# Performance work log

Hardware: AMD Instinct MI355X
Metric: run time of the kernel (lower is better)

## Reference

```python
import jax, jax.numpy as jnp
import numpy as np

N, E = 100000, 1600000
F_IN, F_HID, F_OUT = 64, 64, 16


def setup_inputs() -> dict:
    key = jax.random.key(0)
    ks = jax.random.split(key, 10)
    def g(k, shape):
        return jax.random.normal(k, shape, dtype=jnp.float32) * 0.05
    return {
        "x": jax.random.normal(ks[0], (N, F_IN), dtype=jnp.float32),
        "adj": jax.random.randint(ks[1], (2, E), 0, N, dtype=jnp.int32),
        # ChebConv K=2 params: per-order weights [in, out] + shared bias
        "W1_0": g(ks[2], (F_IN, F_HID)), "W1_1": g(ks[3], (F_IN, F_HID)),
        "b1": jnp.zeros((F_HID,), jnp.float32),
        "Wx_0": g(ks[4], (F_HID, F_HID)), "Wx_1": g(ks[5], (F_HID, F_HID)),
        "bx": jnp.zeros((F_HID,), jnp.float32),
        "W2_0": g(ks[6], (F_HID, F_OUT)), "W2_1": g(ks[7], (F_HID, F_OUT)),
        "b2": jnp.zeros((F_OUT,), jnp.float32),
    }


def _cheb(x, row, col, w, W0, W1, b):
    # K=2 Chebyshev conv: Tx0 = x, Tx1 = L_hat @ x (sparse propagate)
    n = x.shape[0]
    tx1 = jax.ops.segment_sum(w[:, None] * x[col], row, num_segments=n)
    return x @ W0 + tx1 @ W1 + b


def reference(x, adj, W1_0, W1_1, b1, Wx_0, Wx_1, bx, W2_0, W2_1, b2):
    row, col = adj[0], adj[1]
    n = x.shape[0]
    # sym-normalized Laplacian scaled by 2/lambda_max (=1): diagonal cancels,
    # off-diagonal weight = -deg^{-1/2}[row] * deg^{-1/2}[col]
    deg = jax.ops.segment_sum(jnp.ones(adj.shape[1], x.dtype), row, num_segments=n)
    dis = jnp.where(deg > 0, jax.lax.rsqrt(jnp.maximum(deg, 1e-12)), 0.0)
    w = -dis[row] * dis[col]
    h = jax.nn.relu(_cheb(x, row, col, w, W1_0, W1_1, b1))
    # dropout is identity in eval mode
    h = jax.nn.relu(_cheb(h, row, col, w, Wx_0, Wx_1, bx))
    return _cheb(h, row, col, w, W2_0, W2_1, b2)
```

## Files before the change

### kernel.cpp

```cpp
#include <hip/hip_runtime.h>
#include <hip/hip_bf16.h>


#define EPB 4096

typedef __attribute__((ext_vector_type(8))) short bf16x8;
typedef __attribute__((ext_vector_type(4))) float f32x4;

__device__ __forceinline__ float bf2f(unsigned short u) {
    unsigned int x = ((unsigned int)u) << 16;
    return __uint_as_float(x);
}
__device__ __forceinline__ unsigned short f2bf(float f) {
    unsigned int b = __float_as_uint(f);
    unsigned int r = (b + 0x7FFF + ((b >> 16) & 1)) >> 16;
    return (unsigned short)r;
}
__device__ __forceinline__ void acc8(float* a, bf16x8 v) {
#pragma unroll
    for (int i = 0; i < 8; ++i) a[i] += bf2f((unsigned short)(short)v[i]);
}
__device__ __forceinline__ void acc8m(float* a, bf16x8 v, bool m) {
#pragma unroll
    for (int i = 0; i < 8; ++i) a[i] += m ? bf2f((unsigned short)(short)v[i]) : 0.0f;
}

template <int NC>
__device__ __forceinline__ void pack_pair(const float* __restrict__ W0,
                                          const float* __restrict__ W1,
                                          unsigned short* __restrict__ out, int idx) {
    constexpr int NT = NC / 16;
    int i = idx & 7;
    int m = (idx >> 3) & 15;
    int g = (idx >> 7) & 3;
    int f = idx >> 9;
    int nt = f % NT;
    int kt = f / NT;
    const float* W = (kt < 2) ? W0 : W1;
    int k = (kt & 1) * 32 + g * 8 + i;
    out[idx] = f2bf(W[k * NC + nt * 16 + m]);
}

__global__ __launch_bounds__(256) void wconv_all(const float* __restrict__ W1_0,
                                                 const float* __restrict__ W1_1,
                                                 const float* __restrict__ Wx_0,
                                                 const float* __restrict__ Wx_1,
                                                 const float* __restrict__ W2_0,
                                                 const float* __restrict__ W2_1,
                                                 unsigned short* __restrict__ wp1,
                                                 unsigned short* __restrict__ wpx,
                                                 unsigned short* __restrict__ wp2,
                                                 int* __restrict__ bcnt, int nbk) {
    int idx = blockIdx.x * 256 + threadIdx.x;
    if (idx < nbk) bcnt[idx] = 0;
    if (idx < 8192) pack_pair<64>(W1_0, W1_1, wp1, idx);
    else if (idx < 16384) pack_pair<64>(Wx_0, Wx_1, wpx, idx - 8192);
    else if (idx < 18432) pack_pair<16>(W2_0, W2_1, wp2, idx - 16384);
}

__global__ __launch_bounds__(256) void bucket_count(const int* __restrict__ row,
                                                    int* __restrict__ bcnt,
                                                    int e, int nbk) {
    __shared__ int bh[512];
    int tid = threadIdx.x;
    for (int j = tid; j < nbk; j += 256) bh[j] = 0;
    __syncthreads();
    int base = blockIdx.x * EPB;
#pragma unroll
    for (int k = 0; k < EPB / 256; ++k) {
        int i = base + k * 256 + tid;
        if (i < e) atomicAdd(&bh[row[i] >> 8], 1);
    }
    __syncthreads();
    for (int j = tid; j < nbk; j += 256) {
        int c = bh[j];
        if (c) atomicAdd(&bcnt[j], c);
    }
}

__global__ __launch_bounds__(256) void bucket_scan(const int* __restrict__ bcnt,
                                                   int* __restrict__ bbase,
                                                   int* __restrict__ bcursor,
                                                   int* __restrict__ off,
                                                   int nbk, int n, int e) {
    __shared__ int sa[512], sb[512];
    int tid = threadIdx.x;
    for (int j = tid; j < 512; j += 256) sa[j] = (j < nbk) ? bcnt[j] : 0;
    __syncthreads();
    int* in = sa;
    int* out = sb;
    for (int d = 1; d < 512; d <<= 1) {
        for (int j = tid; j < 512; j += 256)
            out[j] = in[j] + ((j >= d) ? in[j - d] : 0);
        __syncthreads();
        int* t = in; in = out; out = t;
    }
    for (int j = tid; j < nbk; j += 256) {
        int incl = in[j];
        int excl = incl - bcnt[j];
        bbase[j] = excl;
        bcursor[j] = excl;
        if (j == nbk - 1) bbase[nbk] = incl;
    }
    if (tid == 0) off[n] = e;
}

__global__ __launch_bounds__(256) void bucket_scatter(const int* __restrict__ row,
                                                      const int* __restrict__ col,
                                                      int* __restrict__ bcursor,
                                                      int* __restrict__ packed,
                                                      int e, int nbk) {
    __shared__ int bh[512];
    __shared__ int bbase[512];
    __shared__ int bcur[512];
    int tid = threadIdx.x;
    for (int j = tid; j < nbk; j += 256) { bh[j] = 0; bcur[j] = 0; }
    __syncthreads();
    int base = blockIdx.x * EPB;
#pragma unroll
    for (int k = 0; k < EPB / 256; ++k) {
        int i = base + k * 256 + tid;
        if (i < e) atomicAdd(&bh[row[i] >> 8], 1);
    }
    __syncthreads();
    for (int j = tid; j < nbk; j += 256) {
        int c = bh[j];
        bbase[j] = c ? atomicAdd(&bcursor[j], c) : 0;
    }
    __syncthreads();
#pragma unroll
    for (int k = 0; k < EPB / 256; ++k) {
        int i = base + k * 256 + tid;
        if (i < e) {
            int r = row[i];
            int b = r >> 8;
            int slot = bbase[b] + atomicAdd(&bcur[b], 1);
            packed[slot] = ((r & 255) << 17) | col[i];
        }
    }
}

__global__ __launch_bounds__(256) void bucket_build(const int* __restrict__ packed,
                                                    const int* __restrict__ bbase,
                                                    const float* __restrict__ x,
                                                    int* __restrict__ off,
                                                    float* __restrict__ dis,
                                                    int* __restrict__ csr,
                                                    unsigned short* __restrict__ y,
                                                    unsigned short* __restrict__ xb,
                                                    int n) {
    __shared__ int rcnt[256];
    __shared__ int sa[256], sb[256];
    __shared__ float disv[256];
    int tid = threadIdx.x;
    int b = blockIdx.x;
    int ebase = bbase[b], eend = bbase[b + 1];
    rcnt[tid] = 0;
    __syncthreads();
    for (int e = ebase + tid; e < eend; e += 256)
        atomicAdd(&rcnt[packed[e] >> 17], 1);
    __syncthreads();
    sa[tid] = rcnt[tid];
    __syncthreads();
    int* in = sa;
    int* out = sb;
    for (int d = 1; d < 256; d <<= 1) {
        out[tid] = in[tid] + ((tid >= d) ? in[tid - d] : 0);
        __syncthreads();
        int* t = in; in = out; out = t;
    }
    int grow = b * 256 + tid;
    int c = rcnt[tid];
    int excl = in[tid] - c;
    float dv = (c > 0) ? rsqrtf((float)c) : 0.0f;
    disv[tid] = dv;
    if (grow < n) {
        off[grow] = ebase + excl;
        dis[grow] = dv;
    }
    out[tid] = excl;
    __syncthreads();
    for (int e = ebase + tid; e < eend; e += 256) {
        int p = packed[e];
        int lr = p >> 17;
        int pos = atomicAdd(&out[lr], 1);
        csr[ebase + pos] = p & 0x1FFFF;
    }
    for (int idx = tid; idx < 4096; idx += 256) {
        int rr = idx >> 4, q = idx & 15;
        int R = b * 256 + rr;
        if (R < n) {
            float d = disv[rr];
            float4 v = ((const float4*)x)[(size_t)R * 16 + q];
            ushort4 o = {f2bf(v.x * d), f2bf(v.y * d), f2bf(v.z * d), f2bf(v.w * d)};
            ((ushort4*)y)[(size_t)R * 16 + q] = o;
            ushort4 xo = {f2bf(v.x), f2bf(v.y), f2bf(v.z), f2bf(v.w)};
            ((ushort4*)xb)[(size_t)R * 16 + q] = xo;
        }
    }
}


template <int NC, bool RELU, bool WRITE_HY>
__global__ __launch_bounds__(256) void agg_dense(const unsigned short* __restrict__ y,
                                                 const unsigned short* __restrict__ A0,
                                                 const int* __restrict__ csr,
                                                 const int* __restrict__ off,
                                                 const float* __restrict__ dis,
                                                 const unsigned short* __restrict__ Wp,
                                                 const float* __restrict__ bias,
                                                 unsigned short* __restrict__ hout,
                                                 unsigned short* __restrict__ yout,
                                                 float* __restrict__ fout,
                                                 int n) {
    constexpr int NT = NC / 16;
    __shared__ unsigned short txl[64 * 64];
    int tid = threadIdx.x;

    int row_l = tid >> 2;
    int fq = tid & 3;
    int r = blockIdx.x * 64 + row_l;
    float acc16[16];
#pragma unroll
    for (int i = 0; i < 16; ++i) acc16[i] = 0.f;
    float d = 0.f;
    if (r < n) {
        int s0 = off[r], e1 = off[r + 1];
        const unsigned short* Yb = y + fq * 16;
        int e1m = e1 - 1;
        for (int t = s0; t < e1; t += 4) {
            int t1 = (t + 1 < e1) ? t + 1 : e1m;
            int t2 = (t + 2 < e1) ? t + 2 : e1m;
            int t3 = (t + 3 < e1) ? t + 3 : e1m;
            int c0 = csr[t], c1 = csr[t1], c2 = csr[t2], c3 = csr[t3];
            const bf16x8* p0 = (const bf16x8*)(Yb + (size_t)c0 * 64);
            const bf16x8* p1 = (const bf16x8*)(Yb + (size_t)c1 * 64);
            const bf16x8* p2 = (const bf16x8*)(Yb + (size_t)c2 * 64);
            const bf16x8* p3 = (const bf16x8*)(Yb + (size_t)c3 * 64);
            bf16x8 v00 = p0[0], v01 = p0[1];
            bf16x8 v10 = p1[0], v11 = p1[1];
            bf16x8 v20 = p2[0], v21 = p2[1];
            bf16x8 v30 = p3[0], v31 = p3[1];
            bool m1 = t + 1 < e1, m2 = t + 2 < e1, m3 = t + 3 < e1;
            acc8(acc16, v00); acc8(acc16 + 8, v01);
            acc8m(acc16, v10, m1); acc8m(acc16 + 8, v11, m1);
            acc8m(acc16, v20, m2); acc8m(acc16 + 8, v21, m2);
            acc8m(acc16, v30, m3); acc8m(acc16 + 8, v31, m3);
        }
        d = -dis[r];
    }
    bf16x8 ov0, ov1;
#pragma unroll
    for (int i = 0; i < 8; ++i) {
        ov0[i] = (short)f2bf(acc16[i] * d);
        ov1[i] = (short)f2bf(acc16[8 + i] * d);
    }
    int swz = (row_l & 7) << 4;
    int cb = fq * 32;
    *(bf16x8*)((char*)txl + row_l * 128 + (cb ^ swz)) = ov0;
    *(bf16x8*)((char*)txl + row_l * 128 + ((cb + 16) ^ swz)) = ov1;
    __syncthreads();

    int lane = tid & 63;
    int m = lane & 15;
    int g = lane >> 4;
    int w = tid >> 6;
    const bf16x8* WP = (const bf16x8*)Wp;
    bf16x8 bf[NT][4];
#pragma unroll
    for (int kt = 0; kt < 4; ++kt)
#pragma unroll
        for (int nt = 0; nt < NT; ++nt)
            bf[nt][kt] = WP[((kt * NT + nt) * 4 + g) * 16 + m];
    int r0 = blockIdx.x * 64 + w * 16;
    int ra = r0 + m;
    if (ra > n - 1) ra = n - 1;
    const unsigned short* q0 = A0 + (size_t)ra * 64 + g * 8;
    bf16x8 a0 = *(const bf16x8*)q0;
    bf16x8 a1 = *(const bf16x8*)(q0 + 32);
    int rl2 = w * 16 + m;
    int sw2 = (m & 7) << 4;
    bf16x8 a2 = *(bf16x8*)((char*)txl + rl2 * 128 + ((g * 16) ^ sw2));
    bf16x8 a3 = *(bf16x8*)((char*)txl + rl2 * 128 + ((64 + g * 16) ^ sw2));
    f32x4 acc[NT];
#pragma unroll
    for (int nt = 0; nt < NT; ++nt) {
        float b = bias[nt * 16 + m];
        acc[nt][0] = b; acc[nt][1] = b; acc[nt][2] = b; acc[nt][3] = b;
    }
#pragma unroll
    for (int nt = 0; nt < NT; ++nt) {
        acc[nt] = __builtin_amdgcn_mfma_f32_16x16x32_bf16(a0, bf[nt][0], acc[nt], 0, 0, 0);
        acc[nt] = __builtin_amdgcn_mfma_f32_16x16x32_bf16(a1, bf[nt][1], acc[nt], 0, 0, 0);
        acc[nt] = __builtin_amdgcn_mfma_f32_16x16x32_bf16(a2, bf[nt][2], acc[nt], 0, 0, 0);
        acc[nt] = __builtin_amdgcn_mfma_f32_16x16x32_bf16(a3, bf[nt][3], acc[nt], 0, 0, 0);
    }
#pragma unroll
    for (int reg = 0; reg < 4; ++reg) {
        int rr = r0 + 4 * g + reg;
        if (rr >= n) continue;
        if (WRITE_HY) {
            float dv = dis[rr];
#pragma unroll
            for (int nt = 0; nt < NT; ++nt) {
                float v = acc[nt][reg];
                if (RELU) v = fmaxf(v, 0.f);
                hout[(size_t)rr * NC + nt * 16 + m] = f2bf(v);
                yout[(size_t)rr * NC + nt * 16 + m] = f2bf(v * dv);
            }
        } else {
#pragma unroll
            for (int nt = 0; nt < NT; ++nt)
                fout[(size_t)rr * NC + nt * 16 + m] = acc[nt][reg];
        }
    }
}


extern "C" void kernel_launch(void* const* d_in, const int* in_sizes, int n_in,
                              void* d_out, int out_size, void* d_ws, size_t ws_size,
                              hipStream_t stream) {
    const float* x    = (const float*)d_in[0];
    const int*   adj  = (const int*)d_in[1];
    const float* W1_0 = (const float*)d_in[2];
    const float* W1_1 = (const float*)d_in[3];
    const float* b1   = (const float*)d_in[4];
    const float* Wx_0 = (const float*)d_in[5];
    const float* Wx_1 = (const float*)d_in[6];
    const float* bx   = (const float*)d_in[7];
    const float* W2_0 = (const float*)d_in[8];
    const float* W2_1 = (const float*)d_in[9];
    const float* b2   = (const float*)d_in[10];
    float* out = (float*)d_out;

    int N = in_sizes[0] / 64;
    int E = in_sizes[1] / 2;
    const int* row = adj;
    const int* col = adj + E;
    int NBK = (N + 255) / 256;

    char* p = (char*)d_ws;
    auto alloc = [&](size_t bytes) {
        char* q = p;
        p += (bytes + 255) & ~(size_t)255;
        return q;
    };
    int*   bcnt  = (int*)alloc((size_t)(NBK) * 4);
    int*   bbase = (int*)alloc((size_t)(NBK + 1) * 4);
    int*   bcur  = (int*)alloc((size_t)(NBK) * 4);
    int*   off   = (int*)alloc((size_t)(N + 1) * 4);
    float* dis   = (float*)alloc((size_t)N * 4);
    int*   csr   = (int*)alloc((size_t)E * 4);
    int*   packed = (int*)alloc((size_t)E * 4);
    unsigned short* wp1 = (unsigned short*)alloc(8192 * 2);
    unsigned short* wpx = (unsigned short*)alloc(8192 * 2);
    unsigned short* wp2 = (unsigned short*)alloc(2048 * 2);
    unsigned short* y  = (unsigned short*)alloc((size_t)N * 64 * 2);
    unsigned short* y2 = (unsigned short*)alloc((size_t)N * 64 * 2);
    unsigned short* xb = (unsigned short*)alloc((size_t)N * 64 * 2);
    unsigned short* h  = (unsigned short*)alloc((size_t)N * 64 * 2);
    unsigned short* h2 = (unsigned short*)alloc((size_t)N * 64 * 2);
    (void)ws_size;

    int EB = (E + EPB - 1) / EPB;
    wconv_all<<<72, 256, 0, stream>>>(W1_0, W1_1, Wx_0, Wx_1, W2_0, W2_1,
                                      wp1, wpx, wp2, bcnt, NBK);
    bucket_count<<<EB, 256, 0, stream>>>(row, bcnt, E, NBK);
    bucket_scan<<<1, 256, 0, stream>>>(bcnt, bbase, bcur, off, NBK, N, E);
    bucket_scatter<<<EB, 256, 0, stream>>>(row, col, bcur, packed, E, NBK);
    bucket_build<<<NBK, 256, 0, stream>>>(packed, bbase, x, off, dis, csr, y, xb, N);

    int nb64 = (N + 63) / 64;
    agg_dense<64, true, true><<<nb64, 256, 0, stream>>>(y, xb, csr, off, dis, wp1, b1, h, y2, nullptr, N);
    agg_dense<64, true, true><<<nb64, 256, 0, stream>>>(y2, h, csr, off, dis, wpx, bx, h2, y, nullptr, N);
    agg_dense<16, false, false><<<nb64, 256, 0, stream>>>(y, h2, csr, off, dis, wp2, b2, nullptr, nullptr, out, N);
}
```

Measured before the change: 185.9 us.

## Project last layer to 16 features before sparse aggregation

```diff
diff --git a/kernel.cpp b/kernel.cpp
--- a/kernel.cpp
+++ b/kernel.cpp
@@ -23,6 +23,15 @@
 __device__ __forceinline__ void acc8m(float* a, bf16x8 v, bool m) {
 #pragma unroll
     for (int i = 0; i < 8; ++i) a[i] += m ? bf2f((unsigned short)(short)v[i]) : 0.0f;
+}
+__device__ __forceinline__ void acc4(float* a, ushort4 v) {
+    a[0] += bf2f(v.x); a[1] += bf2f(v.y); a[2] += bf2f(v.z); a[3] += bf2f(v.w);
+}
+__device__ __forceinline__ void acc4m(float* a, ushort4 v, bool m) {
+    a[0] += m ? bf2f(v.x) : 0.0f;
+    a[1] += m ? bf2f(v.y) : 0.0f;
+    a[2] += m ? bf2f(v.z) : 0.0f;
+    a[3] += m ? bf2f(v.w) : 0.0f;
 }
 
 template <int NC>
@@ -40,6 +49,15 @@
     int k = (kt & 1) * 32 + g * 8 + i;
     out[idx] = f2bf(W[k * NC + nt * 16 + m]);
 }
+__device__ __forceinline__ void pack_single16(const float* __restrict__ W,
+                                              unsigned short* __restrict__ out, int idx) {
+    int i = idx & 7;
+    int m = (idx >> 3) & 15;
+    int g = (idx >> 7) & 3;
+    int kt = idx >> 9;
+    int k = kt * 32 + g * 8 + i;
+    out[idx] = f2bf(W[k * 16 + m]);
+}
 
 __global__ __launch_bounds__(256) void wconv_all(const float* __restrict__ W1_0,
                                                  const float* __restrict__ W1_1,
@@ -49,13 +67,15 @@
                                                  const float* __restrict__ W2_1,
                                                  unsigned short* __restrict__ wp1,
                                                  unsigned short* __restrict__ wpx,
-                                                 unsigned short* __restrict__ wp2,
+                                                 unsigned short* __restrict__ wp2a,
+                                                 unsigned short* __restrict__ wp2b,
                                                  int* __restrict__ bcnt, int nbk) {
     int idx = blockIdx.x * 256 + threadIdx.x;
     if (idx < nbk) bcnt[idx] = 0;
     if (idx < 8192) pack_pair<64>(W1_0, W1_1, wp1, idx);
     else if (idx < 16384) pack_pair<64>(Wx_0, Wx_1, wpx, idx - 8192);
-    else if (idx < 18432) pack_pair<16>(W2_0, W2_1, wp2, idx - 16384);
+    else if (idx < 17408) pack_single16(W2_0, wp2a, idx - 16384);
+    else if (idx < 18432) pack_single16(W2_1, wp2b, idx - 17408);
 }
 
 __global__ __launch_bounds__(256) void bucket_count(const int* __restrict__ row,
@@ -201,7 +221,7 @@
 }
 
 
-template <int NC, bool RELU, bool WRITE_HY>
+template <bool RELU>
 __global__ __launch_bounds__(256) void agg_dense(const unsigned short* __restrict__ y,
                                                  const unsigned short* __restrict__ A0,
                                                  const int* __restrict__ csr,
@@ -211,9 +231,8 @@
                                                  const float* __restrict__ bias,
                                                  unsigned short* __restrict__ hout,
                                                  unsigned short* __restrict__ yout,
-                                                 float* __restrict__ fout,
                                                  int n) {
-    constexpr int NT = NC / 16;
+    constexpr int NT = 4;
     __shared__ unsigned short txl[64 * 64];
     int tid = threadIdx.x;
 
@@ -299,20 +318,126 @@
     for (int reg = 0; reg < 4; ++reg) {
         int rr = r0 + 4 * g + reg;
         if (rr >= n) continue;
-        if (WRITE_HY) {
-            float dv = dis[rr];
-#pragma unroll
-            for (int nt = 0; nt < NT; ++nt) {
-                float v = acc[nt][reg];
-                if (RELU) v = fmaxf(v, 0.f);
-                hout[(size_t)rr * NC + nt * 16 + m] = f2bf(v);
-                yout[(size_t)rr * NC + nt * 16 + m] = f2bf(v * dv);
-            }
-        } else {
-#pragma unroll
-            for (int nt = 0; nt < NT; ++nt)
-                fout[(size_t)rr * NC + nt * 16 + m] = acc[nt][reg];
+        float dv = dis[rr];
+#pragma unroll
+        for (int nt = 0; nt < NT; ++nt) {
+            float v = acc[nt][reg];
+            if (RELU) v = fmaxf(v, 0.f);
+            hout[(size_t)rr * 64 + nt * 16 + m] = f2bf(v);
+            yout[(size_t)rr * 64 + nt * 16 + m] = f2bf(v * dv);
         }
+    }
+}
+
+
+__global__ __launch_bounds__(256) void project16(const unsigned short* __restrict__ y,
+                                                 const unsigned short* __restrict__ Wp,
+                                                 unsigned short* __restrict__ yp,
+                                                 int n, int nrb) {
+    int lane = threadIdx.x & 63;
+    int m = lane & 15;
+    int g = lane >> 4;
+    const bf16x8* WP = (const bf16x8*)Wp;
+    bf16x8 b0 = WP[(0 * 4 + g) * 16 + m];
+    bf16x8 b1 = WP[(1 * 4 + g) * 16 + m];
+    int wrb = blockIdx.x * 4 + (threadIdx.x >> 6);
+    int stride = gridDim.x * 4;
+    for (int rb = wrb; rb < nrb; rb += stride) {
+        int r0 = rb * 16;
+        int ra = r0 + m;
+        if (ra > n - 1) ra = n - 1;
+        const unsigned short* q0 = y + (size_t)ra * 64 + g * 8;
+        bf16x8 a0 = *(const bf16x8*)q0;
+        bf16x8 a1 = *(const bf16x8*)(q0 + 32);
+        f32x4 acc = {0.f, 0.f, 0.f, 0.f};
+        acc = __builtin_amdgcn_mfma_f32_16x16x32_bf16(a0, b0, acc, 0, 0, 0);
+        acc = __builtin_amdgcn_mfma_f32_16x16x32_bf16(a1, b1, acc, 0, 0, 0);
+#pragma unroll
+        for (int reg = 0; reg < 4; ++reg) {
+            int rr = r0 + 4 * g + reg;
+            if (rr < n) yp[(size_t)rr * 16 + m] = f2bf(acc[reg]);
+        }
+    }
+}
+
+
+__global__ __launch_bounds__(256) void agg16(const unsigned short* __restrict__ yp,
+                                             const unsigned short* __restrict__ h2,
+                                             const int* __restrict__ csr,
+                                             const int* __restrict__ off,
+                                             const float* __restrict__ dis,
+                                             const unsigned short* __restrict__ Wp,
+                                             const float* __restrict__ bias,
+                                             float* __restrict__ outp,
+                                             int n) {
+    __shared__ unsigned short t16[64][20];
+    int tid = threadIdx.x;
+
+    int row_l = tid >> 2;
+    int fq = tid & 3;
+    int r = blockIdx.x * 64 + row_l;
+    float a4[4] = {0.f, 0.f, 0.f, 0.f};
+    float d = 0.f;
+    if (r < n) {
+        int s0 = off[r], e1 = off[r + 1];
+        int e1m = e1 - 1;
+        const unsigned short* Yq = yp + fq * 4;
+        for (int t = s0; t < e1; t += 8) {
+            int i1 = (t + 1 < e1) ? t + 1 : e1m;
+            int i2 = (t + 2 < e1) ? t + 2 : e1m;
+            int i3 = (t + 3 < e1) ? t + 3 : e1m;
+            int i4 = (t + 4 < e1) ? t + 4 : e1m;
+            int i5 = (t + 5 < e1) ? t + 5 : e1m;
+            int i6 = (t + 6 < e1) ? t + 6 : e1m;
+            int i7 = (t + 7 < e1) ? t + 7 : e1m;
+            int c0 = csr[t],  c1 = csr[i1], c2 = csr[i2], c3 = csr[i3];
+            int c4 = csr[i4], c5 = csr[i5], c6 = csr[i6], c7 = csr[i7];
+            ushort4 v0 = *(const ushort4*)(Yq + (size_t)c0 * 16);
+            ushort4 v1 = *(const ushort4*)(Yq + (size_t)c1 * 16);
+            ushort4 v2 = *(const ushort4*)(Yq + (size_t)c2 * 16);
+            ushort4 v3 = *(const ushort4*)(Yq + (size_t)c3 * 16);
+            ushort4 v4 = *(const ushort4*)(Yq + (size_t)c4 * 16);
+            ushort4 v5 = *(const ushort4*)(Yq + (size_t)c5 * 16);
+            ushort4 v6 = *(const ushort4*)(Yq + (size_t)c6 * 16);
+            ushort4 v7 = *(const ushort4*)(Yq + (size_t)c7 * 16);
+            bool m1 = t + 1 < e1, m2 = t + 2 < e1, m3 = t + 3 < e1;
+            bool m4 = t + 4 < e1, m5 = t + 5 < e1, m6 = t + 6 < e1, m7 = t + 7 < e1;
+            acc4(a4, v0);
+            acc4m(a4, v1, m1); acc4m(a4, v2, m2); acc4m(a4, v3, m3);
+            acc4m(a4, v4, m4); acc4m(a4, v5, m5); acc4m(a4, v6, m6); acc4m(a4, v7, m7);
+        }
+        d = -dis[r];
+    }
+    ushort4 ov = {f2bf(a4[0] * d), f2bf(a4[1] * d), f2bf(a4[2] * d), f2bf(a4[3] * d)};
+    *(ushort4*)&t16[row_l][fq * 4] = ov;
+    __syncthreads();
+
+    int lane = tid & 63;
+    int m = lane & 15;
+    int g = lane >> 4;
+    int w = tid >> 6;
+    const bf16x8* WP = (const bf16x8*)Wp;
+    bf16x8 b0 = WP[(0 * 4 + g) * 16 + m];
+    bf16x8 b1 = WP[(1 * 4 + g) * 16 + m];
+    int r0 = blockIdx.x * 64 + w * 16;
+    int ra = r0 + m;
+    if (ra > n - 1) ra = n - 1;
+    const unsigned short* q0 = h2 + (size_t)ra * 64 + g * 8;
+    bf16x8 a0 = *(const bf16x8*)q0;
+    bf16x8 a1 = *(const bf16x8*)(q0 + 32);
+    f32x4 acc;
+    {
+        float b = bias[m];
+        acc[0] = b; acc[1] = b; acc[2] = b; acc[3] = b;
+    }
+    acc = __builtin_amdgcn_mfma_f32_16x16x32_bf16(a0, b0, acc, 0, 0, 0);
+    acc = __builtin_amdgcn_mfma_f32_16x16x32_bf16(a1, b1, acc, 0, 0, 0);
+#pragma unroll
+    for (int reg = 0; reg < 4; ++reg) {
+        int rr = r0 + 4 * g + reg;
+        if (rr >= n) continue;
+        int lrow = w * 16 + 4 * g + reg;
+        outp[(size_t)rr * 16 + m] = acc[reg] + bf2f(t16[lrow][m]);
     }
 }
 
@@ -338,6 +463,7 @@
     const int* row = adj;
     const int* col = adj + E;
     int NBK = (N + 255) / 256;
+    int nRB = (N + 15) / 16;
 
     char* p = (char*)d_ws;
     auto alloc = [&](size_t bytes) {
@@ -352,26 +478,29 @@
     float* dis   = (float*)alloc((size_t)N * 4);
     int*   csr   = (int*)alloc((size_t)E * 4);
     int*   packed = (int*)alloc((size_t)E * 4);
-    unsigned short* wp1 = (unsigned short*)alloc(8192 * 2);
-    unsigned short* wpx = (unsigned short*)alloc(8192 * 2);
-    unsigned short* wp2 = (unsigned short*)alloc(2048 * 2);
+    unsigned short* wp1  = (unsigned short*)alloc(8192 * 2);
+    unsigned short* wpx  = (unsigned short*)alloc(8192 * 2);
+    unsigned short* wp2a = (unsigned short*)alloc(1024 * 2);
+    unsigned short* wp2b = (unsigned short*)alloc(1024 * 2);
     unsigned short* y  = (unsigned short*)alloc((size_t)N * 64 * 2);
     unsigned short* y2 = (unsigned short*)alloc((size_t)N * 64 * 2);
     unsigned short* xb = (unsigned short*)alloc((size_t)N * 64 * 2);
     unsigned short* h  = (unsigned short*)alloc((size_t)N * 64 * 2);
     unsigned short* h2 = (unsigned short*)alloc((size_t)N * 64 * 2);
+    unsigned short* yp = (unsigned short*)alloc((size_t)N * 16 * 2);
     (void)ws_size;
 
     int EB = (E + EPB - 1) / EPB;
     wconv_all<<<72, 256, 0, stream>>>(W1_0, W1_1, Wx_0, Wx_1, W2_0, W2_1,
-                                      wp1, wpx, wp2, bcnt, NBK);
+                                      wp1, wpx, wp2a, wp2b, bcnt, NBK);
     bucket_count<<<EB, 256, 0, stream>>>(row, bcnt, E, NBK);
     bucket_scan<<<1, 256, 0, stream>>>(bcnt, bbase, bcur, off, NBK, N, E);
     bucket_scatter<<<EB, 256, 0, stream>>>(row, col, bcur, packed, E, NBK);
     bucket_build<<<NBK, 256, 0, stream>>>(packed, bbase, x, off, dis, csr, y, xb, N);
 
     int nb64 = (N + 63) / 64;
-    agg_dense<64, true, true><<<nb64, 256, 0, stream>>>(y, xb, csr, off, dis, wp1, b1, h, y2, nullptr, N);
-    agg_dense<64, true, true><<<nb64, 256, 0, stream>>>(y2, h, csr, off, dis, wpx, bx, h2, y, nullptr, N);
-    agg_dense<16, false, false><<<nb64, 256, 0, stream>>>(y, h2, csr, off, dis, wp2, b2, nullptr, nullptr, out, N);
-}
+    agg_dense<true><<<nb64, 256, 0, stream>>>(y, xb, csr, off, dis, wp1, b1, h, y2, N);
+    agg_dense<true><<<nb64, 256, 0, stream>>>(y2, h, csr, off, dis, wpx, bx, h2, y, N);
+    project16<<<512, 256, 0, stream>>>(y, wp2b, yp, N, nRB);
+    agg16<<<nb64, 256, 0, stream>>>(yp, h2, csr, off, dis, wp2a, b2, out, N);
+}
```

After: 179.5 us. 3.4% less time.
